# Kernel optimization log

Measured on AMD Instinct MI355X. Metric: run time of the kernel, lower is better.

Reference implementation:

```python
import jax, jax.numpy as jnp
import numpy as np

NUM_HEADS = 16

def _div_no_nan(num, den):
    # TF divide_no_nan semantics: 0 where denominator is 0
    safe = jnp.where(den == 0, 1.0, den)
    return jnp.where(den == 0, 0.0, num / safe)

def setup_inputs() -> dict:
    key = jax.random.key(0)
    x = jax.random.normal(key, (8, 4096, 1024), dtype=jnp.float32)
    return {"x": x}

def reference(x) -> jnp.ndarray:
    B, S, D = x.shape
    H = NUM_HEADS
    hs = D // H
    # [B, S, H, hs] -> [B, H, S, hs]
    t = x.reshape(B, S, H, hs).transpose(0, 2, 1, 3)
    # count_nonzero over the sequence axis (axis=2 here == axis=1 inside _pca)
    non_zeros = jnp.sum((t != 0).astype(jnp.float32), axis=2, keepdims=True)      # [B,H,1,hs]
    zero_vectors = (jnp.sum((t != 0), axis=-1, keepdims=True) > 0).astype(jnp.float32)  # [B,H,S,1]
    mean_vector = _div_no_nan(jnp.sum(t, axis=2, keepdims=True), non_zeros)       # [B,H,1,hs]
    var_vector = jnp.sum(_div_no_nan(jnp.square(t - mean_vector), non_zeros), axis=2, keepdims=True)
    std_vector = jnp.sqrt(var_vector)                                             # [B,H,1,hs]
    out = _div_no_nan(t - mean_vector, std_vector) * zero_vectors                 # [B,H,S,hs]
    # Gram matrix per (batch, head): [B,H,hs,hs]
    gram = jnp.einsum('bhsi,bhsj->bhij', out, out)
    eigen_values, eigen_vectors = jnp.linalg.eigh(gram)      # [B,H,hs], [B,H,hs,hs]
    # diag(w) @ V then transpose the last two axes
    pca = jnp.swapaxes(eigen_values[..., :, None] * eigen_vectors, -1, -2)        # [B,H,hs,hs]
    pca = pca.reshape(B, H * hs, hs)
    return pca / jnp.sqrt(jnp.asarray(hs, dtype=jnp.float32))
```

## Files before the change

kernel.cpp:

```cpp
#include <hip/hip_runtime.h>
#include <math.h>


#define NMAT 128
#define EPS32 5.9604644775390625e-8
#define SAFMIN32 1.1754943508222875e-38

static __device__ __forceinline__ double f32r(double x) { return (double)(float)x; }
static __device__ __forceinline__ double lapsign(double a, double b) {
  return (b >= 0.0) ? fabs(a) : -fabs(a);
}

__device__ __forceinline__ double wred_sum(double v) {
#pragma unroll
  for (int o = 32; o > 0; o >>= 1) v += __shfl_xor(v, o, 64);
  return v;
}
__device__ __forceinline__ double wred_max(double v) {
#pragma unroll
  for (int o = 32; o > 0; o >>= 1) v = fmax(v, __shfl_xor(v, o, 64));
  return v;
}

__global__ __launch_bounds__(256) void gram_kernel(const float* __restrict__ x,
                                                   float* __restrict__ gbuf) {
  const int bh = blockIdx.x, b = bh >> 4, h = bh & 15;
  const float* base = x + (size_t)b * 4096 * 1024 + h * 64;
  __shared__ double rs1[16][64];
  __shared__ double rs2[16][64];
  __shared__ int rsc[16][64];
  __shared__ float sm[64], si[64];
  __shared__ double tiled[2][64][68];
  const int tid = threadIdx.x, q = tid & 15, r0 = tid >> 4, lane = tid & 63;

  double s1[4] = {0.0, 0.0, 0.0, 0.0}, s2[4] = {0.0, 0.0, 0.0, 0.0};
  int cc[4] = {0, 0, 0, 0};
#pragma unroll 4
  for (int s = r0; s < 4096; s += 16) {
    const float4 v = *(const float4*)&base[(size_t)s * 1024 + 4 * q];
    const float vs[4] = {v.x, v.y, v.z, v.w};
#pragma unroll
    for (int k = 0; k < 4; ++k) {
      const double dv = (double)vs[k];
      s1[k] += dv;
      s2[k] += dv * dv;
      cc[k] += (vs[k] != 0.0f) ? 1 : 0;
    }
  }
#pragma unroll
  for (int k = 0; k < 4; ++k) {
    rs1[r0][4 * q + k] = s1[k];
    rs2[r0][4 * q + k] = s2[k];
    rsc[r0][4 * q + k] = cc[k];
  }
  __syncthreads();
  if (tid < 64) {
    double S1 = 0.0, S2 = 0.0;
    int C = 0;
    for (int a = 0; a < 16; ++a) { S1 += rs1[a][tid]; S2 += rs2[a][tid]; C += rsc[a][tid]; }
    const double m = (C > 0) ? S1 / (double)C : 0.0;
    double var = (C > 0) ? (S2 - 2.0 * m * S1 + 4096.0 * m * m) / (double)C : 0.0;
    var = fmax(var, 0.0);
    const double sd = sqrt(var);
    sm[tid] = (float)m;
    si[tid] = (sd > 0.0) ? (float)(1.0 / sd) : 0.0f;
  }
  __syncthreads();

  const float4 mj4 = *(const float4*)&sm[4 * q];
  const float4 iv4 = *(const float4*)&si[4 * q];

  auto stash = [&](int buf, const float4& v, int sl) {
    const bool nz4 = (v.x != 0.0f) || (v.y != 0.0f) || (v.z != 0.0f) || (v.w != 0.0f);
    const unsigned long long mb = __ballot(nz4);
    const unsigned rowm = (unsigned)(mb >> (lane & 48)) & 0xFFFFu;
    double* tr = &tiled[buf][sl][4 * q];
    if (rowm) {
      tr[0] = (double)((v.x - mj4.x) * iv4.x);
      tr[1] = (double)((v.y - mj4.y) * iv4.y);
      tr[2] = (double)((v.z - mj4.z) * iv4.z);
      tr[3] = (double)((v.w - mj4.w) * iv4.w);
    } else {
      tr[0] = 0.0; tr[1] = 0.0; tr[2] = 0.0; tr[3] = 0.0;
    }
  };

  double acc[4][4];
#pragma unroll
  for (int r = 0; r < 4; ++r)
#pragma unroll
    for (int c = 0; c < 4; ++c) acc[r][c] = 0.0;

  {
    const float4 p0 = *(const float4*)&base[(size_t)(r0) * 1024 + 4 * q];
    const float4 p1 = *(const float4*)&base[(size_t)(r0 + 16) * 1024 + 4 * q];
    const float4 p2 = *(const float4*)&base[(size_t)(r0 + 32) * 1024 + 4 * q];
    const float4 p3 = *(const float4*)&base[(size_t)(r0 + 48) * 1024 + 4 * q];
    stash(0, p0, r0); stash(0, p1, r0 + 16); stash(0, p2, r0 + 32); stash(0, p3, r0 + 48);
  }
  __syncthreads();

  for (int t = 0; t < 64; ++t) {
    const int cur = t & 1;
    float4 n0, n1, n2, n3;
    const bool more = (t + 1 < 64);
    if (more) {
      const size_t sb = (size_t)(t + 1) * 64;
      n0 = *(const float4*)&base[(sb + r0) * 1024 + 4 * q];
      n1 = *(const float4*)&base[(sb + r0 + 16) * 1024 + 4 * q];
      n2 = *(const float4*)&base[(sb + r0 + 32) * 1024 + 4 * q];
      n3 = *(const float4*)&base[(sb + r0 + 48) * 1024 + 4 * q];
    }
    for (int ss = 0; ss < 64; ++ss) {
      const double* ta = &tiled[cur][ss][4 * r0];
      const double* tb = &tiled[cur][ss][4 * q];
      const double a0 = ta[0], a1 = ta[1], a2 = ta[2], a3 = ta[3];
      const double b0 = tb[0], b1 = tb[1], b2 = tb[2], b3 = tb[3];
      acc[0][0] += a0 * b0; acc[0][1] += a0 * b1; acc[0][2] += a0 * b2; acc[0][3] += a0 * b3;
      acc[1][0] += a1 * b0; acc[1][1] += a1 * b1; acc[1][2] += a1 * b2; acc[1][3] += a1 * b3;
      acc[2][0] += a2 * b0; acc[2][1] += a2 * b1; acc[2][2] += a2 * b2; acc[2][3] += a2 * b3;
      acc[3][0] += a3 * b0; acc[3][1] += a3 * b1; acc[3][2] += a3 * b2; acc[3][3] += a3 * b3;
    }
    if (more) {
      stash(cur ^ 1, n0, r0); stash(cur ^ 1, n1, r0 + 16);
      stash(cur ^ 1, n2, r0 + 32); stash(cur ^ 1, n3, r0 + 48);
    }
    __syncthreads();
  }

  float* G = gbuf + (size_t)bh * 4096;
#pragma unroll
  for (int r = 0; r < 4; ++r)
#pragma unroll
    for (int c = 0; c < 4; ++c)
      G[(4 * r0 + r) * 64 + 4 * q + c] = (float)acc[r][c];
}

static __device__ void dlartg_d(double f, double g, double& cs, double& sn,
                                double& r) {
  if (g == 0.0) { cs = 1.0; sn = 0.0; r = f; }
  else if (f == 0.0) { cs = 0.0; sn = 1.0; r = g; }
  else {
    r = sqrt(f * f + g * g);
    cs = f / r; sn = g / r;
    if (fabs(f) > fabs(g) && cs < 0.0) { cs = -cs; sn = -sn; r = -r; }
  }
}

static __device__ void dlaev2_d(double a, double b, double c, double& rt1,
                                double& rt2, double& cs1, double& sn1) {
  double sm = a + c, df = a - c, adf = fabs(df), tb = b + b, ab = fabs(tb);
  double acmx, acmn;
  if (fabs(a) > fabs(c)) { acmx = a; acmn = c; } else { acmx = c; acmn = a; }
  double rt;
  if (adf > ab) rt = adf * sqrt(1.0 + (ab / adf) * (ab / adf));
  else if (adf < ab) rt = ab * sqrt(1.0 + (adf / ab) * (adf / ab));
  else rt = ab * sqrt(2.0);
  int sgn1;
  if (sm < 0.0) {
    rt1 = 0.5 * (sm - rt); sgn1 = -1;
    rt2 = (acmx / rt1) * acmn - (b / rt1) * b;
  } else if (sm > 0.0) {
    rt1 = 0.5 * (sm + rt); sgn1 = 1;
    rt2 = (acmx / rt1) * acmn - (b / rt1) * b;
  } else { rt1 = 0.5 * rt; rt2 = -0.5 * rt; sgn1 = 1; }
  int sgn2; double cs;
  if (df >= 0.0) { cs = df + rt; sgn2 = 1; } else { cs = df - rt; sgn2 = -1; }
  double acs = fabs(cs);
  if (acs > ab) {
    double ct = -tb / cs;
    sn1 = 1.0 / sqrt(1.0 + ct * ct); cs1 = ct * sn1;
  } else {
    if (ab == 0.0) { cs1 = 1.0; sn1 = 0.0; }
    else {
      double tn = -cs / tb;
      cs1 = 1.0 / sqrt(1.0 + tn * tn); sn1 = tn * cs1;
    }
  }
  if (sgn1 == sgn2) { double tn = cs1; cs1 = -sn1; sn1 = tn; }
}

static __device__ __forceinline__ void rot1(double (*Zs)[65], int base, int row,
                                            int k1, int k2, double c, double s) {
  double a = Zs[base + row][base + k1], b = Zs[base + row][base + k2];
  Zs[base + row][base + k1] = c * a + s * b;
  Zs[base + row][base + k2] = -s * a + c * b;
}

static __device__ void dsteqr16_coop(double* d, double* e, double (*Zs)[65],
                                     int base, int row, double* cw, double* sw) {
  const int n = 16, nm1 = 15;
  const double eps = EPS32, eps2 = EPS32 * EPS32;
  int l1 = 0, jtot = 0, nmaxit = n * 30;
  while (l1 < n) {
    if (l1 > 0) e[l1 - 1] = 0.0;
    int m;
    for (m = l1; m < nm1; ++m) {
      double tst = fabs(e[m]);
      if (tst == 0.0) break;
      if (tst <= (sqrt(fabs(d[m])) * sqrt(fabs(d[m + 1]))) * eps) {
        e[m] = 0.0; break;
      }
    }
    int l = l1, lend = m;
    l1 = m + 1;
    if (lend == l) continue;
    if (fabs(d[lend]) < fabs(d[l])) { int t = l; l = lend; lend = t; }
    if (lend > l) {
      for (;;) {
        int mm;
        if (l != lend) {
          for (mm = l; mm < lend; ++mm) {
            double tst = e[mm] * e[mm];
            if (tst <= (eps2 * fabs(d[mm])) * fabs(d[mm + 1]) + SAFMIN32) break;
          }
        } else mm = lend;
        if (mm < lend) e[mm] = 0.0;
        double p = d[l];
        if (mm == l) { d[l] = p; ++l; if (l <= lend) continue; else break; }
        if (mm == l + 1) {
          double rt1, rt2, c, s;
          dlaev2_d(d[l], e[l], d[l + 1], rt1, rt2, c, s);
          rot1(Zs, base, row, l, l + 1, c, s);
          d[l] = rt1; d[l + 1] = rt2; e[l] = 0.0;
          l += 2; if (l <= lend) continue; else break;
        }
        if (jtot == nmaxit) break;
        ++jtot;
        double g = (d[l + 1] - p) / (2.0 * e[l]);
        double r = sqrt(g * g + 1.0);
        g = d[mm] - p + e[l] / (g + lapsign(r, g));
        double s = 1.0, c = 1.0; p = 0.0;
        for (int i = mm - 1; i >= l; --i) {
          double f = s * e[i], b = c * e[i];
          dlartg_d(g, f, c, s, r);
          if (i != mm - 1) e[i + 1] = r;
          g = d[i + 1] - p;
          r = (d[i] - g) * s + 2.0 * c * b;
          p = s * r;
          d[i + 1] = g + p;
          g = c * r - b;
          cw[i] = c; sw[i] = -s;
        }
        for (int k = mm - 1; k >= l; --k) rot1(Zs, base, row, k, k + 1, cw[k], sw[k]);
        d[l] -= p; e[l] = g;
      }
    } else {
      for (;;) {
        int mm;
        if (l != lend) {
          for (mm = l; mm > lend; --mm) {
            double tst = e[mm - 1] * e[mm - 1];
            if (tst <= (eps2 * fabs(d[mm])) * fabs(d[mm - 1]) + SAFMIN32) break;
          }
        } else mm = lend;
        if (mm > lend) e[mm - 1] = 0.0;
        double p = d[l];
        if (mm == l) { d[l] = p; --l; if (l >= lend) continue; else break; }
        if (mm == l - 1) {
          double rt1, rt2, c, s;
          dlaev2_d(d[l - 1], e[l - 1], d[l], rt1, rt2, c, s);
          rot1(Zs, base, row, l - 1, l, c, s);
          d[l - 1] = rt1; d[l] = rt2; e[l - 1] = 0.0;
          l -= 2; if (l >= lend) continue; else break;
        }
        if (jtot == nmaxit) break;
        ++jtot;
        double g = (d[l - 1] - p) / (2.0 * e[l - 1]);
        double r = sqrt(g * g + 1.0);
        g = d[mm] - p + e[l - 1] / (g + lapsign(r, g));
        double s = 1.0, c = 1.0; p = 0.0;
        for (int i = mm; i <= l - 1; ++i) {
          double f = s * e[i], b = c * e[i];
          dlartg_d(g, f, c, s, r);
          if (i != mm) e[i - 1] = r;
          g = d[i] - p;
          r = (d[i + 1] - g) * s + 2.0 * c * b;
          p = s * r;
          d[i] = g + p;
          g = c * r - b;
          cw[i] = c; sw[i] = s;
        }
        for (int k = mm; k <= l - 1; ++k) rot1(Zs, base, row, k, k + 1, cw[k], sw[k]);
        d[l] -= p; e[l - 1] = g;
      }
    }
  }
  for (int ii = 1; ii < n; ++ii) {
    int i = ii - 1, k = i; double p = d[i];
    for (int j = ii; j < n; ++j)
      if (d[j] < p) { k = j; p = d[j]; }
    if (k != i) {
      d[k] = d[i]; d[i] = p;
      double t = Zs[base + row][base + i];
      Zs[base + row][base + i] = Zs[base + row][base + k];
      Zs[base + row][base + k] = t;
    }
  }
}

static __device__ void merge_dc(int off, int n, double rho_in, int lane,
                                double (*Zs)[65], double (*Zn)[65], float* ScF,
                                double* dd, double* dlam, double* wz,
                                double* zt, double* lamv, double* zloc,
                                double* dloc, double* lamfin, double* dvalS,
                                double* rz2, int* indx, int* slist, int* dlist,
                                int* dcolS) {
  const int N1 = n / 2;
  if (lane < n) {
    int r = (lane < N1) ? (off + N1 - 1) : (off + N1);
    double z = Zs[r][off + lane];
    if (rho_in < 0.0 && lane >= N1) z = -z;
    zloc[lane] = z * 0.70710678118654752440;
    dloc[lane] = dd[off + lane];
  }
  __syncthreads();
  const double rho = fabs(2.0 * rho_in);
  if (lane < n) {
    double a = dloc[lane];
    int pos;
    if (lane < N1) {
      int c2 = 0;
      for (int i = N1; i < n; ++i) c2 += (dloc[i] < a) ? 1 : 0;
      pos = lane + c2;
    } else {
      int c1 = 0;
      for (int i = 0; i < N1; ++i) c1 += (dloc[i] <= a) ? 1 : 0;
      pos = (lane - N1) + c1;
    }
    indx[pos] = lane;
  }
  __syncthreads();
  double mx = (lane < n) ? fmax(fabs(dloc[lane]), fabs(zloc[lane])) : 0.0;
  mx = wred_max(mx);
  const double tol = 8.0 * EPS32 * mx;
  __syncthreads();

  int K = 0, nD = 0;
  {
    int pj = -1, j = 0;
    for (; j < n; ++j) {
      int cj = indx[j];
      if (rho * fabs(zloc[cj]) <= tol) { dlist[nD] = cj; ++nD; }
      else { pj = cj; ++j; break; }
    }
    if (pj >= 0) {
      for (; j < n; ++j) {
        int nj = indx[j];
        if (rho * fabs(zloc[nj]) <= tol) { dlist[nD] = nj; ++nD; continue; }
        double s0 = zloc[pj], c0 = zloc[nj];
        double ta = sqrt(c0 * c0 + s0 * s0);
        double tt = dloc[nj] - dloc[pj];
        double cc = c0 / ta, ss = -s0 / ta;
        if (fabs(tt * cc * ss) <= tol) {
          zloc[nj] = ta; zloc[pj] = 0.0;
          {
            double a = Zs[lane][off + pj], b = Zs[lane][off + nj];
            Zs[lane][off + pj] = cc * a + ss * b;
            Zs[lane][off + nj] = cc * b - ss * a;
          }
          double ndp = dloc[pj] * cc * cc + dloc[nj] * ss * ss;
          dloc[nj] = dloc[pj] * ss * ss + dloc[nj] * cc * cc;
          dloc[pj] = ndp;
          dlist[nD] = pj; ++nD;
          pj = nj;
        } else {
          slist[K] = pj; ++K;
          pj = nj;
        }
      }
      slist[K] = pj; ++K;
    }
  }
  __syncthreads();
  if (lane == 0) {
    for (int m = 0; m < nD; ++m) { dvalS[m] = dloc[dlist[m]]; dcolS[m] = dlist[m]; }
    for (int a = 1; a < nD; ++a) {
      double v = dvalS[a]; int ci = dcolS[a]; int b = a - 1;
      while (b >= 0 && dvalS[b] > v) { dvalS[b+1] = dvalS[b]; dcolS[b+1] = dcolS[b]; --b; }
      dvalS[b+1] = v; dcolS[b+1] = ci;
    }
  }
  __syncthreads();
  if (lane < K) {
    const double dv = dloc[slist[lane]], zv = zloc[slist[lane]];
    dlam[lane] = dv; wz[lane] = zv; rz2[lane] = rho * (zv * zv);
  }
  __syncthreads();

  if (lane < K) {
    int jl = lane, pjp; double lo, hi;
    double sumz2 = 0.0;
    for (int i = 0; i < K; ++i) sumz2 += wz[i] * wz[i];
    if (jl < K - 1) {
      double mid = 0.5 * (dlam[jl] + dlam[jl + 1]);
      double f = 1.0;
      for (int i = 0; i < K; ++i) f += rho * wz[i] * wz[i] / (dlam[i] - mid);
      double gaph = 0.5 * (dlam[jl + 1] - dlam[jl]);
      if (f > 0.0) { pjp = jl;     lo = 0.0;   hi = gaph; }
      else         { pjp = jl + 1; lo = -gaph; hi = 0.0;  }
    } else { pjp = K - 1; lo = 0.0; hi = rho * sumz2; }
    double sig = dlam[pjp];
    double tau = 0.5 * (lo + hi);
    for (int it = 0; it < 100; ++it) {
      double g = 1.0, gp = 0.0;
      for (int i = 0; i < K; ++i) {
        double inv = 1.0 / ((dlam[i] - sig) - tau);
        double q = rz2[i] * inv;
        g += q;
        gp += q * inv;
      }
      if (g > 0.0) hi = tau; else lo = tau;
      double tn = tau - g / gp;
      if (!(tn > lo && tn < hi)) tn = 0.5 * (lo + hi);
      double df = fabs(tn - tau);
      tau = tn;
      if (df <= 1.0e-12 * (fabs(tau) + 1e-30)) break;
    }
    lamv[jl] = sig + tau;
    for (int i = 0; i < K; ++i)
      ScF[i * 65 + jl] = (float)((dlam[i] - sig) - tau);
  }
  __syncthreads();
  if (lane < K) {
    int i = lane;
    double wv = (double)ScF[i * 65 + i];
    for (int j2 = 0; j2 < K; ++j2) {
      if (j2 == i) continue;
      wv *= (double)ScF[i * 65 + j2] / (dlam[i] - dlam[j2]);
    }
    double mag = sqrt(fmax(-wv, 0.0));
    zt[i] = (wz[i] >= 0.0) ? mag : -mag;
  }
  __syncthreads();
  if (lane < K) {
    double nrm2 = 0.0;
    for (int i = 0; i < K; ++i) {
      double sv = zt[i] / (double)ScF[i * 65 + lane];
      ScF[i * 65 + lane] = (float)sv;
      nrm2 += sv * sv;
    }
    float inv = (float)(1.0 / sqrt(nrm2));
    for (int i = 0; i < K; ++i) ScF[i * 65 + lane] *= inv;
  }
  __syncthreads();
  if (lane < K) {
    int cnt = 0;
    for (int m = 0; m < nD; ++m) cnt += (dvalS[m] < lamv[lane]) ? 1 : 0;
    int fp = lane + cnt;
    for (int c0 = 0; c0 < n; c0 += 16) {
      double res[16];
#pragma unroll
      for (int t = 0; t < 16; ++t) res[t] = 0.0;
      for (int i = 0; i < K; ++i) {
        double sv = (double)ScF[i * 65 + lane];
        int col = off + slist[i];
#pragma unroll
        for (int t = 0; t < 16; ++t) res[t] += Zs[off + c0 + t][col] * sv;
      }
#pragma unroll
      for (int t = 0; t < 16; ++t) Zn[c0 + t][fp] = res[t];
    }
    lamfin[fp] = lamv[lane];
  }
  __syncthreads();
  for (int m = 0; m < nD; ++m) {
    int cnt = 0;
    for (int jl = 0; jl < K; ++jl) cnt += (lamv[jl] <= dvalS[m]) ? 1 : 0;
    int fp = m + cnt;
    if (lane < n) Zn[lane][fp] = Zs[off + lane][off + dcolS[m]];
    if (lane == 0) lamfin[fp] = dvalS[m];
  }
  __syncthreads();
  if (lane < n) {
    for (int c = 0; c < n; ++c) Zs[off + lane][off + c] = Zn[lane][c];
    dd[off + lane] = f32r(lamfin[lane]);
  }
  __syncthreads();
}

__global__ __launch_bounds__(64, 1) void eig_kernel(float* __restrict__ gbuf) {
  const int bh = blockIdx.x, b = bh >> 4, h = bh & 15;
  const int lane = threadIdx.x;
  float* G = gbuf + (size_t)bh * 4096;

  __shared__ double Zs[64][65];
  __shared__ double Zn[64][65];
  __shared__ double varch[64][64];
  __shared__ double ScD[2080];
  __shared__ double dd[64], ee[64], tauv[64], varr[64], wv[64];
  __shared__ double dlam[64], wz[64], zt[64], lamv[64], zloc[64], dloc[64];
  __shared__ double lamfin[64], dvalS[64], dsave[64], esave[64], rz2[64];
  __shared__ double cwA[4][16], swA[4][16];
  __shared__ int indx[64], slist[64], dlist[64], dcolS[64];
  float* ScF = (float*)ScD;

  double (*Zw)[65] = Zs;
  for (int r = 0; r < 64; ++r) Zw[r][lane] = (double)G[r * 64 + lane];
  __syncthreads();

  for (int i = 0; i < 63; ++i) {
    double xv = (lane >= i + 2) ? Zw[i][lane] : 0.0;
    double xn2 = wred_sum(xv * xv);
    double alpha = Zw[i][i + 1];
    double beta, taui;
    if (xn2 == 0.0) { taui = 0.0; beta = alpha; }
    else {
      double nrm = sqrt(alpha * alpha + xn2);
      beta = (alpha >= 0.0) ? -nrm : nrm;
      taui = (beta - alpha) / beta;
    }
    if (lane == 0) { dd[i] = Zw[i][i]; ee[i] = beta; tauv[i] = taui; }
    if (taui != 0.0) {
      double vl = (lane == i + 1) ? 1.0
                                  : ((lane >= i + 2) ? xv / (alpha - beta) : 0.0);
      varr[lane] = vl;
      if (lane >= i + 1) varch[i][lane] = vl;
      __syncthreads();
      double wr = 0.0;
      for (int c = i + 1; c < 64; ++c) wr += Zw[c][lane] * varr[c];
      wr *= taui;
      double wtv = wred_sum((lane >= i + 1) ? wr * vl : 0.0);
      wr -= 0.5 * taui * wtv * vl;
      wv[lane] = (lane >= i + 1) ? wr : 0.0;
      __syncthreads();
      if (lane >= i + 1) {
        double vc = vl, wc = wr;
        for (int r = i + 1; r < 64; ++r)
          Zw[r][lane] -= (varr[r] * wc + wv[r] * vc);
      }
      __syncthreads();
    } else {
      __syncthreads();
    }
  }
  if (lane == 0) dd[63] = Zw[63][63];
  __syncthreads();

  dd[lane] = f32r(dd[lane]);
  if (lane < 63) ee[lane] = f32r(ee[lane]);
  __syncthreads();
  double mx = fabs(dd[lane]);
  if (lane < 63) mx = fmax(mx, fabs(ee[lane]));
  const double orgnrm = wred_max(mx);
  dd[lane] = f32r(dd[lane] / orgnrm);
  if (lane < 63) ee[lane] = f32r(ee[lane] / orgnrm);
  __syncthreads();
  dsave[lane] = dd[lane];
  esave[lane] = (lane < 63) ? ee[lane] : 0.0;
  __syncthreads();
  if (lane == 0) {
    const int ms[3] = {15, 31, 47};
    for (int a = 0; a < 3; ++a) {
      double ae = fabs(ee[ms[a]]);
      dd[ms[a]] = f32r(dd[ms[a]] - ae);
      dd[ms[a] + 1] = f32r(dd[ms[a] + 1] - ae);
    }
  }
  __syncthreads();

  for (int r = 0; r < 64; ++r) Zs[r][lane] = (r == lane) ? 1.0 : 0.0;
  __syncthreads();
  {
    const int bb = lane >> 4, row = lane & 15;
    dsteqr16_coop(dd + bb * 16, ee + bb * 16, Zs, bb * 16, row, cwA[bb], swA[bb]);
  }
  __syncthreads();
  dd[lane] = f32r(dd[lane]);
  __syncthreads();

  merge_dc(0, 32, ee[15], lane, Zs, Zn, ScF, dd, dlam, wz, zt, lamv, zloc,
           dloc, lamfin, dvalS, rz2, indx, slist, dlist, dcolS);
  merge_dc(32, 32, ee[47], lane, Zs, Zn, ScF, dd, dlam, wz, zt, lamv, zloc,
           dloc, lamfin, dvalS, rz2, indx, slist, dlist, dcolS);
  merge_dc(0, 64, ee[31], lane, Zs, Zn, ScF, dd, dlam, wz, zt, lamv, zloc,
           dloc, lamfin, dvalS, rz2, indx, slist, dlist, dcolS);

  double tres = 0.0;
  {
    const double lam = dd[lane];
    for (int i = 0; i < 64; ++i) {
      double tv = dsave[i] * Zs[i][lane];
      if (i > 0) tv += esave[i - 1] * Zs[i - 1][lane];
      if (i < 63) tv += esave[i] * Zs[i + 1][lane];
      tres = fmax(tres, fabs(tv - lam * Zs[i][lane]));
    }
  }
  tres = wred_max(tres);
  const bool dc_bad = !(tres <= 2e-5);

  for (int i = 62; i >= 0; --i) {
    double ti = tauv[i];
    if (ti != 0.0) {
      varr[lane] = varch[i][lane];
      __syncthreads();
      double wc = 0.0;
      for (int r = i + 1; r < 64; ++r) wc += varr[r] * Zs[r][lane];
      wc *= ti;
      for (int r = i + 1; r < 64; ++r) Zs[r][lane] -= varr[r] * wc;
      __syncthreads();
    }
  }
  __syncthreads();

  const double sentinel = dc_bad ? 1.0e6 : 0.0;
  const double wj = dd[lane] * orgnrm * 0.125;
  for (int i2 = 0; i2 < 64; ++i2) {
    G[i2 * 64 + lane] = (float)(wj * Zs[lane][i2] + sentinel);
  }
}

extern "C" void kernel_launch(void* const* d_in, const int* in_sizes, int n_in,
                              void* d_out, int out_size, void* d_ws,
                              size_t ws_size, hipStream_t stream) {
  (void)in_sizes; (void)n_in; (void)out_size; (void)d_ws; (void)ws_size;
  const float* x = (const float*)d_in[0];
  float* out = (float*)d_out;
  gram_kernel<<<dim3(NMAT), dim3(256), 0, stream>>>(x, out);
  eig_kernel<<<dim3(NMAT), dim3(64), 0, stream>>>(out);
}
```

Baseline: 1.759 ms.

## Keep tridiagonal QL state in registers with shuffles and ballot-based deflation search

Rewrites the 16x16 tridiagonal QL solver so that each lane holds its own diagonal and off-diagonal entries in registers rather than in shared arrays. Neighbouring values are exchanged with shuffles, and the deflation search becomes a ballot plus find-first-set instead of a serial loop. The Givens rotations are applied to the eigenvector row in the same loop through a carry variable, which removes the stored cos/sin arrays and the separate rotation pass. The final sort uses shuffle min-reductions. The cost is many more shuffles per iteration, and the mixed 16-lane-group control flow must stay uniform within each group.

```diff
diff --git a/kernel.cpp b/kernel.cpp
--- a/kernel.cpp
+++ b/kernel.cpp
@@ -180,118 +180,159 @@
   if (sgn1 == sgn2) { double tn = cs1; cs1 = -sn1; sn1 = tn; }
 }
 
-static __device__ __forceinline__ void rot1(double (*Zs)[65], int base, int row,
-                                            int k1, int k2, double c, double s) {
-  double a = Zs[base + row][base + k1], b = Zs[base + row][base + k2];
-  Zs[base + row][base + k1] = c * a + s * b;
-  Zs[base + row][base + k2] = -s * a + c * b;
-}
-
-static __device__ void dsteqr16_coop(double* d, double* e, double (*Zs)[65],
-                                     int base, int row, double* cw, double* sw) {
+static __device__ void dsteqr16_grp(double (*Zs)[65], int base, int lane,
+                                    double& dk, double& ek) {
   const int n = 16, nm1 = 15;
   const double eps = EPS32, eps2 = EPS32 * EPS32;
+  const int gb = lane & 48;
+  const int row = lane & 15;
   int l1 = 0, jtot = 0, nmaxit = n * 30;
   while (l1 < n) {
-    if (l1 > 0) e[l1 - 1] = 0.0;
+    if (l1 > 0) { if (row == l1 - 1) ek = 0.0; }
     int m;
-    for (m = l1; m < nm1; ++m) {
-      double tst = fabs(e[m]);
-      if (tst == 0.0) break;
-      if (tst <= (sqrt(fabs(d[m])) * sqrt(fabs(d[m + 1]))) * eps) {
-        e[m] = 0.0; break;
-      }
+    {
+      double dkp1 = __shfl(dk, gb + ((row + 1) & 15));
+      bool cond = (fabs(ek) <= (sqrt(fabs(dk)) * sqrt(fabs(dkp1))) * eps);
+      unsigned grp = (unsigned)((__ballot(cond) >> gb) & 0xFFFFull);
+      grp &= 0x7FFFu & ~((1u << l1) - 1);
+      m = grp ? (__ffs(grp) - 1) : nm1;
+      if (m < nm1) { if (row == m) ek = 0.0; }
     }
     int l = l1, lend = m;
     l1 = m + 1;
     if (lend == l) continue;
-    if (fabs(d[lend]) < fabs(d[l])) { int t = l; l = lend; lend = t; }
+    if (fabs(__shfl(dk, gb + lend)) < fabs(__shfl(dk, gb + l))) {
+      int t = l; l = lend; lend = t;
+    }
     if (lend > l) {
       for (;;) {
         int mm;
-        if (l != lend) {
-          for (mm = l; mm < lend; ++mm) {
-            double tst = e[mm] * e[mm];
-            if (tst <= (eps2 * fabs(d[mm])) * fabs(d[mm + 1]) + SAFMIN32) break;
-          }
-        } else mm = lend;
-        if (mm < lend) e[mm] = 0.0;
-        double p = d[l];
-        if (mm == l) { d[l] = p; ++l; if (l <= lend) continue; else break; }
+        {
+          double dkp1 = __shfl(dk, gb + ((row + 1) & 15));
+          bool cond = (ek * ek <= (eps2 * fabs(dk)) * fabs(dkp1) + SAFMIN32);
+          unsigned grp = (unsigned)((__ballot(cond) >> gb) & 0xFFFFull);
+          unsigned rng = ((1u << lend) - 1) & ~((1u << l) - 1);
+          grp &= rng;
+          mm = grp ? (__ffs(grp) - 1) : lend;
+        }
+        if (mm < lend) { if (row == mm) ek = 0.0; }
+        double p = __shfl(dk, gb + l);
+        if (mm == l) { ++l; if (l <= lend) continue; else break; }
         if (mm == l + 1) {
           double rt1, rt2, c, s;
-          dlaev2_d(d[l], e[l], d[l + 1], rt1, rt2, c, s);
-          rot1(Zs, base, row, l, l + 1, c, s);
-          d[l] = rt1; d[l + 1] = rt2; e[l] = 0.0;
+          dlaev2_d(__shfl(dk, gb + l), __shfl(ek, gb + l),
+                   __shfl(dk, gb + l + 1), rt1, rt2, c, s);
+          {
+            double a = Zs[base + row][base + l], b = Zs[base + row][base + l + 1];
+            Zs[base + row][base + l] = c * a + s * b;
+            Zs[base + row][base + l + 1] = -s * a + c * b;
+          }
+          if (row == l) { dk = rt1; ek = 0.0; }
+          if (row == l + 1) dk = rt2;
           l += 2; if (l <= lend) continue; else break;
         }
         if (jtot == nmaxit) break;
         ++jtot;
-        double g = (d[l + 1] - p) / (2.0 * e[l]);
+        double el = __shfl(ek, gb + l);
+        double g = (__shfl(dk, gb + l + 1) - p) / (2.0 * el);
         double r = sqrt(g * g + 1.0);
-        g = d[mm] - p + e[l] / (g + lapsign(r, g));
+        g = __shfl(dk, gb + mm) - p + el / (g + lapsign(r, g));
         double s = 1.0, c = 1.0; p = 0.0;
+        double carry = 0.0;
+        bool first = true;
         for (int i = mm - 1; i >= l; --i) {
-          double f = s * e[i], b = c * e[i];
+          double za = Zs[base + row][base + i];
+          double ei = __shfl(ek, gb + i);
+          double f = s * ei, b = c * ei;
           dlartg_d(g, f, c, s, r);
-          if (i != mm - 1) e[i + 1] = r;
-          g = d[i + 1] - p;
-          r = (d[i] - g) * s + 2.0 * c * b;
+          if (i != mm - 1) { if (row == i + 1) ek = r; }
+          g = __shfl(dk, gb + i + 1) - p;
+          r = (__shfl(dk, gb + i) - g) * s + 2.0 * c * b;
           p = s * r;
-          d[i + 1] = g + p;
+          if (row == i + 1) dk = g + p;
           g = c * r - b;
-          cw[i] = c; sw[i] = -s;
+          double zb = first ? Zs[base + row][base + i + 1] : carry;
+          Zs[base + row][base + i + 1] = s * za + c * zb;
+          carry = c * za - s * zb;
+          first = false;
         }
-        for (int k = mm - 1; k >= l; --k) rot1(Zs, base, row, k, k + 1, cw[k], sw[k]);
-        d[l] -= p; e[l] = g;
+        Zs[base + row][base + l] = carry;
+        if (row == l) { dk -= p; ek = g; }
       }
     } else {
       for (;;) {
         int mm;
-        if (l != lend) {
-          for (mm = l; mm > lend; --mm) {
-            double tst = e[mm - 1] * e[mm - 1];
-            if (tst <= (eps2 * fabs(d[mm])) * fabs(d[mm - 1]) + SAFMIN32) break;
-          }
-        } else mm = lend;
-        if (mm > lend) e[mm - 1] = 0.0;
-        double p = d[l];
-        if (mm == l) { d[l] = p; --l; if (l >= lend) continue; else break; }
+        {
+          int lm1 = (row == 0) ? 0 : row - 1;
+          double dkm1 = __shfl(dk, gb + lm1);
+          double ekm1 = __shfl(ek, gb + lm1);
+          bool cond = (ekm1 * ekm1 <= (eps2 * fabs(dk)) * fabs(dkm1) + SAFMIN32);
+          unsigned grp = (unsigned)((__ballot(cond) >> gb) & 0xFFFFull);
+          unsigned rng = ((1u << (l + 1)) - 1) & ~((1u << (lend + 1)) - 1);
+          grp &= rng;
+          mm = grp ? (31 - __clz(grp)) : lend;
+        }
+        if (mm > lend) { if (row == mm - 1) ek = 0.0; }
+        double p = __shfl(dk, gb + l);
+        if (mm == l) { --l; if (l >= lend) continue; else break; }
         if (mm == l - 1) {
           double rt1, rt2, c, s;
-          dlaev2_d(d[l - 1], e[l - 1], d[l], rt1, rt2, c, s);
-          rot1(Zs, base, row, l - 1, l, c, s);
-          d[l - 1] = rt1; d[l] = rt2; e[l - 1] = 0.0;
+          dlaev2_d(__shfl(dk, gb + l - 1), __shfl(ek, gb + l - 1),
+                   __shfl(dk, gb + l), rt1, rt2, c, s);
+          {
+            double a = Zs[base + row][base + l - 1], b = Zs[base + row][base + l];
+            Zs[base + row][base + l - 1] = c * a + s * b;
+            Zs[base + row][base + l] = -s * a + c * b;
+          }
+          if (row == l - 1) { dk = rt1; ek = 0.0; }
+          if (row == l) dk = rt2;
           l -= 2; if (l >= lend) continue; else break;
         }
         if (jtot == nmaxit) break;
         ++jtot;
-        double g = (d[l - 1] - p) / (2.0 * e[l - 1]);
+        double elm1 = __shfl(ek, gb + l - 1);
+        double g = (__shfl(dk, gb + l - 1) - p) / (2.0 * elm1);
         double r = sqrt(g * g + 1.0);
-        g = d[mm] - p + e[l - 1] / (g + lapsign(r, g));
+        g = __shfl(dk, gb + mm) - p + elm1 / (g + lapsign(r, g));
         double s = 1.0, c = 1.0; p = 0.0;
+        double carry = 0.0;
+        bool first = true;
         for (int i = mm; i <= l - 1; ++i) {
-          double f = s * e[i], b = c * e[i];
+          double zb = Zs[base + row][base + i + 1];
+          double ei = __shfl(ek, gb + i);
+          double f = s * ei, b = c * ei;
           dlartg_d(g, f, c, s, r);
-          if (i != mm) e[i - 1] = r;
-          g = d[i] - p;
-          r = (d[i + 1] - g) * s + 2.0 * c * b;
+          if (i != mm) { if (row == i - 1) ek = r; }
+          g = __shfl(dk, gb + i) - p;
+          r = (__shfl(dk, gb + i + 1) - g) * s + 2.0 * c * b;
           p = s * r;
-          d[i] = g + p;
+          if (row == i) dk = g + p;
           g = c * r - b;
-          cw[i] = c; sw[i] = s;
+          double za = first ? Zs[base + row][base + i] : carry;
+          Zs[base + row][base + i] = c * za + s * zb;
+          carry = -s * za + c * zb;
+          first = false;
         }
-        for (int k = mm; k <= l - 1; ++k) rot1(Zs, base, row, k, k + 1, cw[k], sw[k]);
-        d[l] -= p; e[l - 1] = g;
+        Zs[base + row][base + l] = carry;
+        if (row == l) dk -= p;
+        if (row == l - 1) ek = g;
       }
     }
   }
   for (int ii = 1; ii < n; ++ii) {
-    int i = ii - 1, k = i; double p = d[i];
-    for (int j = ii; j < n; ++j)
-      if (d[j] < p) { k = j; p = d[j]; }
-    if (k != i) {
-      d[k] = d[i]; d[i] = p;
+    int i = ii - 1;
+    double p = __shfl(dk, gb + i);
+    double mv = (row >= ii) ? dk : 1.0e300;
+    mv = fmin(mv, __shfl_xor(mv, 8));
+    mv = fmin(mv, __shfl_xor(mv, 4));
+    mv = fmin(mv, __shfl_xor(mv, 2));
+    mv = fmin(mv, __shfl_xor(mv, 1));
+    if (mv < p) {
+      unsigned grp = (unsigned)((__ballot(row >= ii && dk == mv) >> gb) & 0xFFFFull);
+      int k = __ffs(grp) - 1;
+      double dko = __shfl(dk, gb + k);
+      if (row == k) dk = p;
+      if (row == i) dk = dko;
       double t = Zs[base + row][base + i];
       Zs[base + row][base + i] = Zs[base + row][base + k];
       Zs[base + row][base + k] = t;
@@ -491,7 +532,6 @@
   __shared__ double dd[64], ee[64], tauv[64], varr[64], wv[64];
   __shared__ double dlam[64], wz[64], zt[64], lamv[64], zloc[64], dloc[64];
   __shared__ double lamfin[64], dvalS[64], dsave[64], esave[64], rz2[64];
-  __shared__ double cwA[4][16], swA[4][16];
   __shared__ int indx[64], slist[64], dlist[64], dcolS[64];
   float* ScF = (float*)ScD;
 
@@ -562,8 +602,11 @@
   for (int r = 0; r < 64; ++r) Zs[r][lane] = (r == lane) ? 1.0 : 0.0;
   __syncthreads();
   {
-    const int bb = lane >> 4, row = lane & 15;
-    dsteqr16_coop(dd + bb * 16, ee + bb * 16, Zs, bb * 16, row, cwA[bb], swA[bb]);
+    const int bb = lane >> 4, row16 = lane & 15;
+    double dk = dd[bb * 16 + row16];
+    double ek = (row16 < 15) ? ee[bb * 16 + row16] : 0.0;
+    dsteqr16_grp(Zs, bb * 16, lane, dk, ek);
+    dd[bb * 16 + row16] = dk;
   }
   __syncthreads();
   dd[lane] = f32r(dd[lane]);
```

Measured after the change: 1.683 ms. 1.05x faster.
